# Performance work log

Hardware: AMD Instinct MI355X
Metric: run time of the kernel (lower is better)

## Reference

```python
import jax, jax.numpy as jnp
import numpy as np

B, L, D, H = 32, 512, 512, 8          # batch(=num_nodes), seq len, model_size, num_heads
HD = D // H                            # head size
E_DIM, N_EDGES, N_PATHS = 128, 4096, 1024  # edge_dim (hardcoded 128), edge table, #(src,dst) pairs
MAXD = H                               # max_path_distance == num_heads


def setup_inputs() -> dict:
    rng = jax.random.key(0)
    ks = jax.random.split(rng, 16)
    n = lambda k, s: jax.random.normal(k, s, jnp.float32)
    idx = jnp.arange(N_PATHS)
    inp = {
        'query': n(ks[0], (B, L, D)),
        'key':   n(ks[1], (B, L, D)),
        'value': n(ks[2], (B, L, D)),
        'mask':  jnp.ones((B, 1, 1, L), jnp.float32),
        'edge_attr': n(ks[3], (N_EDGES, E_DIM)),
        'path_src': (idx // B).astype(jnp.int32),   # all (src,dst) node pairs
        'path_dst': (idx % B).astype(jnp.int32),
        'path_edges': jax.random.randint(ks[4], (N_PATHS, MAXD), 0, N_EDGES),
        'path_lens': jax.random.randint(ks[5], (N_PATHS,), 1, MAXD + 1),
        # learned params
        'WQ': n(ks[6], (D, D)) * 0.02, 'bQ': jnp.zeros((D,), jnp.float32),
        'WK': n(ks[7], (D, D)) * 0.02, 'bK': jnp.zeros((D,), jnp.float32),
        'WV': n(ks[8], (D, D)) * 0.02, 'bV': jnp.zeros((D,), jnp.float32),
        'WO': n(ks[9], (D, D)) * 0.02, 'bO': jnp.zeros((D,), jnp.float32),
        'edge_vector': n(ks[10], (MAXD, E_DIM)) * 0.05,  # EdgeEncoding weight
        'b_vec': n(ks[11], (MAXD,)) * 0.05,              # SpatialEncoding weight
        'b_scale': jnp.float32(0.001),
        'c_scale': jnp.float32(0.001),
    }
    return inp


def reference(query, key, value, mask, edge_attr, path_src, path_dst, path_edges,
              path_lens, WQ, bQ, WK, bK, WV, bV, WO, bO, edge_vector, b_vec,
              b_scale, c_scale):
    def split_heads(x):  # [B,L,D] -> [B,H,L,HD]
        return x.reshape(B, L, H, HD).transpose(0, 2, 1, 3)

    q = split_heads(jnp.einsum('bld,de->ble', query, WQ) + bQ)
    k = split_heads(jnp.einsum('bld,de->ble', key, WK) + bK)
    v = split_heads(jnp.einsum('bld,de->ble', value, WV) + bV)

    score = jnp.einsum('bhqd,bhkd->bhqk', q, k) / jnp.sqrt(jnp.float32(HD))

    pl = jnp.minimum(path_lens, MAXD).astype(jnp.int32)  # clipped path lengths

    # SpatialEncoding: spatial[src,dst] = b_vec[min(len,maxd)-1]
    spatial = jnp.zeros((B, B), jnp.float32).at[path_src, path_dst].set(b_vec[pl - 1])
    b_mean = spatial.mean(axis=1)  # [B]

    # EdgeEncoding: cij[src,dst] = mean_k <edge_vector[k], edge_attr[path[k]]>
    pe = edge_attr[path_edges]                       # [P,MAXD,E]  batched gather
    dots = jnp.einsum('ke,pke->pk', edge_vector, pe)  # [P,MAXD]
    kmask = (jnp.arange(MAXD)[None, :] < pl[:, None]).astype(jnp.float32)
    cvals = jnp.where(pl > 0, (dots * kmask).sum(1) / jnp.maximum(pl, 1), 0.0)
    cij = jnp.zeros((B, B), jnp.float32).at[path_src, path_dst].set(cvals)
    c_mean = cij.mean(axis=1)  # [B]

    bias = (b_scale * b_mean + c_scale * c_mean)[:, None, None, None]
    score = score + bias + (1.0 - mask) * (-1e9)

    alpha = jax.nn.softmax(score, axis=-1)
    ctx = jnp.einsum('bhqk,bhkd->bhqd', alpha, v)
    ctx = ctx.transpose(0, 2, 1, 3).reshape(B, L, D)
    return jnp.einsum('bld,de->ble', ctx, WO) + bO
```

## Files before the change

kernel.cpp:

```cpp
#include <hip/hip_runtime.h>
#include <hip/hip_bf16.h>

#define B_  32
#define L_  512
#define D_  512
#define H_  8
#define HD_ 64

typedef __attribute__((ext_vector_type(8))) short bf16x8;
typedef __attribute__((ext_vector_type(4))) short bf16x4;
typedef __attribute__((ext_vector_type(4))) float f32x4;

__device__ __forceinline__ short f2bf(float f) {
  union { float f; unsigned u; } x; x.f = f;
  unsigned r = x.u + 0x7FFFu + ((x.u >> 16) & 1u);
  return (short)(r >> 16);
}

__device__ __forceinline__ void gll16(const void* g, void* l) {
  __builtin_amdgcn_global_load_lds(
      (const __attribute__((address_space(1))) unsigned int*)g,
      (__attribute__((address_space(3))) unsigned int*)l, 16, 0, 0);
}

__device__ __forceinline__ bf16x8 cvt8(f32x4 a, f32x4 b) {
  union { __hip_bfloat162 h[4]; bf16x8 v; } u;
  u.h[0] = __float22bfloat162_rn(float2{a[0], a[1]});
  u.h[1] = __float22bfloat162_rn(float2{a[2], a[3]});
  u.h[2] = __float22bfloat162_rn(float2{b[0], b[1]});
  u.h[3] = __float22bfloat162_rn(float2{b[2], b[3]});
  return u.v;
}

#define DS_FENCE() do { asm volatile("s_waitcnt lgkmcnt(0)" ::: "memory"); \
                        __builtin_amdgcn_sched_barrier(0); } while (0)

__global__ __launch_bounds__(256) void wt_kernel(
    const float* __restrict__ WQ, const float* __restrict__ WK,
    const float* __restrict__ WV, const float* __restrict__ WO,
    short* __restrict__ wt) {
  __shared__ float tile[32][33];
  int wz = blockIdx.z;
  const float* W = (wz == 0) ? WQ : (wz == 1) ? WK : (wz == 2) ? WV : WO;
  int k0 = blockIdx.y * 32, n0 = blockIdx.x * 32;
  int tr = threadIdx.x >> 5, tc = threadIdx.x & 31;
#pragma unroll
  for (int i = 0; i < 4; ++i)
    tile[tr + i * 8][tc] = W[(size_t)(k0 + tr + i * 8) * D_ + n0 + tc];
  __syncthreads();
#pragma unroll
  for (int i = 0; i < 4; ++i)
    wt[((size_t)wz * D_ + n0 + tr + i * 8) * D_ + k0 + tc] =
        f2bf(tile[tc][tr + i * 8]);
}

__global__ __launch_bounds__(256, 4) void gemm_qkv(
    const float* __restrict__ Xq, const float* __restrict__ Xk,
    const float* __restrict__ Xv, const short* __restrict__ wt,
    const float* __restrict__ bQ, const float* __restrict__ bK,
    const float* __restrict__ bV,
    short* __restrict__ q_ws, short* __restrict__ k_ws,
    short* __restrict__ vt_ws) {
  __shared__ __align__(16) char lds[32768];
  char* Al = lds;
  char* Bl = lds + 16384;

  int mode = blockIdx.z;
  const float* A = (mode == 0) ? Xq : (mode == 1) ? Xk : Xv;
  const short* WT = wt + (size_t)mode * D_ * D_;
  const float* bias = (mode == 0) ? bQ : (mode == 1) ? bK : bV;

  int wgid = blockIdx.x + 4 * blockIdx.y;
  int xcd = wgid & 7, idx = wgid >> 3;
  int m0 = (xcd * 32 + (idx >> 2)) * 64;
  int n0 = (idx & 3) * 128;

  int tid = threadIdx.x, lane = tid & 63, w = tid >> 6;
  int wr = w >> 1, wc = w & 1, g = lane >> 4, lr = lane & 15;

  f32x4 acc[2][4] = {};

#pragma unroll
  for (int ks = 0; ks < 8; ++ks) {
    __syncthreads();
#pragma unroll
    for (int j = 0; j < 4; ++j) {
      int e = w * 4 + j;
      int row = e * 4 + (lane >> 4);
      int chunk = (lane & 15) ^ (row & 15);
      gll16(A + (size_t)(m0 + row) * D_ + ks * 64 + chunk * 4, Al + e * 1024);
    }
#pragma unroll
    for (int j = 0; j < 4; ++j) {
      int e = w * 4 + j;
      int row = e * 8 + (lane >> 3);
      int chunk = (lane & 7) ^ (lane >> 3);
      gll16(WT + (size_t)(n0 + row) * D_ + ks * 64 + chunk * 8, Bl + e * 1024);
    }
    __syncthreads();
#pragma unroll
    for (int kk = 0; kk < 2; ++kk) {
      bf16x8 af[2], bf_[4];
#pragma unroll
      for (int i = 0; i < 2; ++i) {
        int row = wr * 32 + i * 16 + lr;
        int o0 = ((kk * 8 + g * 2) ^ lr) << 4;
        int o1 = ((kk * 8 + g * 2 + 1) ^ lr) << 4;
        f32x4 lo = *(const f32x4*)(Al + row * 256 + o0);
        f32x4 hi = *(const f32x4*)(Al + row * 256 + o1);
        af[i] = cvt8(lo, hi);
      }
#pragma unroll
      for (int i = 0; i < 4; ++i) {
        int row = wc * 64 + i * 16 + lr;
        bf_[i] = *(const bf16x8*)(Bl + row * 128 +
                                  (((kk * 4 + g) ^ (lr & 7)) << 4));
      }
#pragma unroll
      for (int mi = 0; mi < 2; ++mi)
#pragma unroll
        for (int nj = 0; nj < 4; ++nj)
          acc[mi][nj] = __builtin_amdgcn_mfma_f32_16x16x32_bf16(
              af[mi], bf_[nj], acc[mi][nj], 0, 0, 0);
    }
  }

#pragma unroll
  for (int mi = 0; mi < 2; ++mi) {
#pragma unroll
    for (int nj = 0; nj < 4; ++nj) {
      int n = n0 + wc * 64 + nj * 16 + lr;
      float bb = bias[n];
      int h = n >> 6, hd = n & 63;
#pragma unroll
      for (int rr = 0; rr < 4; ++rr) {
        int m = m0 + wr * 32 + mi * 16 + g * 4 + rr;
        int b = m >> 9, l = m & 511;
        short v = f2bf(acc[mi][nj][rr] + bb);
        if (mode == 0)
          q_ws[(((size_t)b * H_ + h) * L_ + l) * HD_ + hd] = v;
        else if (mode == 1)
          k_ws[(((size_t)b * H_ + h) * L_ + l) * HD_ + hd] = v;
        else
          vt_ws[(((size_t)b * H_ + h) * HD_ + hd) * L_ + l] = v;
      }
    }
  }
}

__global__ __launch_bounds__(256, 4) void attn_kernel(
    const short* __restrict__ q_ws, const short* __restrict__ k_ws,
    const short* __restrict__ vt_ws, const float* __restrict__ mask,
    short* __restrict__ ctx_ws) {
  __shared__ __align__(16) char lds[40960];
  int wg = blockIdx.x;
  int bh   = (wg & 7) * 32 + (wg >> 6);
  int qblk = (wg >> 3) & 7;
  int b = bh >> 3, h = bh & 7;
  int tid = threadIdx.x, lane = tid & 63, w = tid >> 6;
  int g = lane >> 4, lr = lane & 15;
  char* Pl = lds + 32768 + w * 2048;
  int qbase = qblk * 64 + w * 16;

  const short* Qh  = q_ws  + (size_t)bh * (L_ * HD_);
  const short* Kh  = k_ws  + (size_t)bh * (L_ * HD_);
  const short* VTh = vt_ws + (size_t)bh * (HD_ * L_);
  const float* mrow = mask + (size_t)b * L_;

  bf16x8 aq0 = *(const bf16x8*)(Qh + (size_t)(qbase + lr) * HD_ + g * 8);
  bf16x8 aq1 = *(const bf16x8*)(Qh + (size_t)(qbase + lr) * HD_ + 32 + g * 8);

  float mb_all[32];
#pragma unroll
  for (int ch = 0; ch < 8; ++ch)
#pragma unroll
    for (int kt = 0; kt < 4; ++kt)
      mb_all[ch * 4 + kt] = (1.0f - mrow[ch * 64 + kt * 16 + lr]) * -1e9f;

  int rowin = lane >> 3;
  int sch8 = ((lane & 7) ^ rowin) * 8;

#pragma unroll
  for (int j = 0; j < 2; ++j) {
    int e = w * 2 + j, row = e * 8 + rowin;
    gll16(Kh + (size_t)row * HD_ + sch8, lds + e * 1024);
    gll16(VTh + (size_t)row * L_ + sch8, lds + 16384 + e * 1024);
  }
  __syncthreads();

  f32x4 c[4] = {};
  float m[4] = {-1e30f, -1e30f, -1e30f, -1e30f};
  float sum[4] = {0.f, 0.f, 0.f, 0.f};

#pragma unroll
  for (int ch = 0; ch < 8; ++ch) {
    const char* Kb = lds + (ch & 1) * 8192;
    const char* Vb = lds + 16384 + (ch & 1) * 8192;
    if (ch < 7) {
      char* Kn = lds + ((ch + 1) & 1) * 8192;
      char* Vn = lds + 16384 + ((ch + 1) & 1) * 8192;
#pragma unroll
      for (int j = 0; j < 2; ++j) {
        int e = w * 2 + j, row = e * 8 + rowin;
        gll16(Kh + ((size_t)(ch + 1) * 64 + row) * HD_ + sch8, Kn + e * 1024);
        gll16(VTh + (size_t)row * L_ + (ch + 1) * 64 + sch8, Vn + e * 1024);
      }
    }

    f32x4 s[4];
    __builtin_amdgcn_s_setprio(1);
#pragma unroll
    for (int kt = 0; kt < 4; ++kt) {
      int row = kt * 16 + lr;
      bf16x8 bk0 = *(const bf16x8*)(Kb + row * 128 + ((g ^ (lr & 7)) << 4));
      bf16x8 bk1 = *(const bf16x8*)(Kb + row * 128 + (((4 + g) ^ (lr & 7)) << 4));
      f32x4 a = {0.f, 0.f, 0.f, 0.f};
      a = __builtin_amdgcn_mfma_f32_16x16x32_bf16(aq0, bk0, a, 0, 0, 0);
      a = __builtin_amdgcn_mfma_f32_16x16x32_bf16(aq1, bk1, a, 0, 0, 0);
#pragma unroll
      for (int rr = 0; rr < 4; ++rr)
        a[rr] = a[rr] * 0.125f + mb_all[ch * 4 + kt];
      s[kt] = a;
    }
    __builtin_amdgcn_s_setprio(0);

    float pmax[4];
#pragma unroll
    for (int rr = 0; rr < 4; ++rr)
      pmax[rr] = fmaxf(fmaxf(s[0][rr], s[1][rr]), fmaxf(s[2][rr], s[3][rr]));
#pragma unroll
    for (int off = 1; off < 16; off <<= 1)
#pragma unroll
      for (int rr = 0; rr < 4; ++rr)
        pmax[rr] = fmaxf(pmax[rr], __shfl_xor(pmax[rr], off, 64));

    int ok = (pmax[0] - m[0] <= 8.f) & (pmax[1] - m[1] <= 8.f) &
             (pmax[2] - m[2] <= 8.f) & (pmax[3] - m[3] <= 8.f);
    if (!__all(ok)) {
      float scl[4];
#pragma unroll
      for (int rr = 0; rr < 4; ++rr) {
        float mn = fmaxf(m[rr], pmax[rr]);
        scl[rr] = __expf(m[rr] - mn);
        m[rr] = mn;
        sum[rr] *= scl[rr];
      }
#pragma unroll
      for (int nt = 0; nt < 4; ++nt)
#pragma unroll
        for (int rr = 0; rr < 4; ++rr) c[nt][rr] *= scl[rr];
    }

#pragma unroll
    for (int kt = 0; kt < 4; ++kt) {
      int col2 = (kt * 16 + lr) * 2;
#pragma unroll
      for (int rr = 0; rr < 4; ++rr) {
        float p = __expf(s[kt][rr] - m[rr]);
        sum[rr] += p;
        int row = g * 4 + rr;
        *(short*)(Pl + row * 128 + (col2 ^ ((row & 7) << 4))) = f2bf(p);
      }
    }
    DS_FENCE();

    __builtin_amdgcn_s_setprio(1);
#pragma unroll
    for (int kk = 0; kk < 2; ++kk) {
      bf16x8 ap = *(const bf16x8*)(Pl + lr * 128 +
                                   (((kk * 4 + g) ^ (lr & 7)) << 4));
#pragma unroll
      for (int nt = 0; nt < 4; ++nt) {
        int row = nt * 16 + lr;
        bf16x8 bv = *(const bf16x8*)(Vb + row * 128 +
                                     (((kk * 4 + g) ^ (lr & 7)) << 4));
        c[nt] = __builtin_amdgcn_mfma_f32_16x16x32_bf16(ap, bv, c[nt], 0, 0, 0);
      }
    }
    __builtin_amdgcn_s_setprio(0);
    DS_FENCE();
    if (ch < 7) __syncthreads();
  }

  float inv[4];
#pragma unroll
  for (int off = 1; off < 16; off <<= 1)
#pragma unroll
    for (int rr = 0; rr < 4; ++rr) sum[rr] += __shfl_xor(sum[rr], off, 64);
#pragma unroll
  for (int rr = 0; rr < 4; ++rr) inv[rr] = 1.0f / sum[rr];

#pragma unroll
  for (int nt = 0; nt < 4; ++nt) {
    int hd = nt * 16 + lr;
#pragma unroll
    for (int rr = 0; rr < 4; ++rr) {
      int qrow = qbase + g * 4 + rr;
      ctx_ws[(((size_t)b * L_ + qrow) * H_ + h) * HD_ + hd] =
          f2bf(c[nt][rr] * inv[rr]);
    }
  }
}

__global__ __launch_bounds__(256, 4) void gemm_out(
    const short* __restrict__ ctx, const short* __restrict__ wt3,
    const float* __restrict__ bO, float* __restrict__ out) {
  __shared__ __align__(16) char lds[24576];
  char* Al = lds;
  char* Bl = lds + 8192;
  int wgid = blockIdx.x + 4 * blockIdx.y;
  int xcd = wgid & 7, idx = wgid >> 3;
  int m0 = (xcd * 32 + (idx >> 2)) * 64;
  int n0 = (idx & 3) * 128;
  int tid = threadIdx.x, lane = tid & 63, w = tid >> 6;
  int wr = w >> 1, wc = w & 1, g = lane >> 4, lr = lane & 15;

  f32x4 acc[2][4] = {};

#pragma unroll
  for (int ks = 0; ks < 8; ++ks) {
    __syncthreads();
#pragma unroll
    for (int j = 0; j < 2; ++j) {
      int e = w * 2 + j;
      int row = e * 8 + (lane >> 3);
      int chunk = (lane & 7) ^ (lane >> 3);
      gll16(ctx + (size_t)(m0 + row) * D_ + ks * 64 + chunk * 8, Al + e * 1024);
    }
#pragma unroll
    for (int j = 0; j < 4; ++j) {
      int e = w * 4 + j;
      int row = e * 8 + (lane >> 3);
      int chunk = (lane & 7) ^ (lane >> 3);
      gll16(wt3 + (size_t)(n0 + row) * D_ + ks * 64 + chunk * 8, Bl + e * 1024);
    }
    __syncthreads();
#pragma unroll
    for (int kk = 0; kk < 2; ++kk) {
      bf16x8 af[2], bf_[4];
#pragma unroll
      for (int i = 0; i < 2; ++i) {
        int row = wr * 32 + i * 16 + lr;
        af[i] = *(const bf16x8*)(Al + row * 128 +
                                 (((kk * 4 + g) ^ (lr & 7)) << 4));
      }
#pragma unroll
      for (int i = 0; i < 4; ++i) {
        int row = wc * 64 + i * 16 + lr;
        bf_[i] = *(const bf16x8*)(Bl + row * 128 +
                                  (((kk * 4 + g) ^ (lr & 7)) << 4));
      }
#pragma unroll
      for (int mi = 0; mi < 2; ++mi)
#pragma unroll
        for (int nj = 0; nj < 4; ++nj)
          acc[mi][nj] = __builtin_amdgcn_mfma_f32_16x16x32_bf16(
              af[mi], bf_[nj], acc[mi][nj], 0, 0, 0);
    }
  }
#pragma unroll
  for (int mi = 0; mi < 2; ++mi) {
#pragma unroll
    for (int nj = 0; nj < 4; ++nj) {
      int n = n0 + wc * 64 + nj * 16 + lr;
      float bb = bO[n];
#pragma unroll
      for (int rr = 0; rr < 4; ++rr) {
        int m = m0 + wr * 32 + mi * 16 + g * 4 + rr;
        out[(size_t)m * D_ + n] = acc[mi][nj][rr] + bb;
      }
    }
  }
}

extern "C" void kernel_launch(void* const* d_in, const int* in_sizes, int n_in,
                              void* d_out, int out_size, void* d_ws,
                              size_t ws_size, hipStream_t stream) {
  const float* query = (const float*)d_in[0];
  const float* key   = (const float*)d_in[1];
  const float* value = (const float*)d_in[2];
  const float* mask  = (const float*)d_in[3];
  const float* WQ = (const float*)d_in[9];
  const float* bQ = (const float*)d_in[10];
  const float* WK = (const float*)d_in[11];
  const float* bK = (const float*)d_in[12];
  const float* WV = (const float*)d_in[13];
  const float* bV = (const float*)d_in[14];
  const float* WO = (const float*)d_in[15];
  const float* bO = (const float*)d_in[16];

  short* ws  = (short*)d_ws;
  short* wt  = ws;
  short* q   = ws + 1048576;
  short* k   = q + 8388608;
  short* vt  = k + 8388608;
  short* ctx = vt + 8388608;
  float* out = (float*)d_out;

  wt_kernel<<<dim3(16, 16, 4), 256, 0, stream>>>(WQ, WK, WV, WO, wt);
  gemm_qkv<<<dim3(4, 256, 3), 256, 0, stream>>>(query, key, value, wt,
                                                bQ, bK, bV, q, k, vt);
  attn_kernel<<<2048, 256, 0, stream>>>(q, k, vt, mask, ctx);
  gemm_out<<<dim3(4, 256), 256, 0, stream>>>(ctx, wt + 3 * 262144, bO, out);
}
```

Measured before the change: 130.9 us.

## Load QKV GEMM A operand directly to registers with register prefetch

The fp32 activation tile in the QKV projection GEMM is no longer staged through LDS. Each lane now loads its A fragment straight from global memory into registers and prefetches the next k-step while the current one computes. This removes the A-side LDS traffic and halves the LDS footprint, which may allow higher occupancy. In exchange it uses more registers, and the per-lane global loads are less coalesced, since rows are read by different lanes and each row is read by both column-warps.

```diff
diff --git a/kernel.cpp b/kernel.cpp
--- a/kernel.cpp
+++ b/kernel.cpp
@@ -61,9 +61,7 @@
     const float* __restrict__ bV,
     short* __restrict__ q_ws, short* __restrict__ k_ws,
     short* __restrict__ vt_ws) {
-  __shared__ __align__(16) char lds[32768];
-  char* Al = lds;
-  char* Bl = lds + 16384;
+  __shared__ __align__(16) char Bl[16384];
 
   int mode = blockIdx.z;
   const float* A = (mode == 0) ? Xq : (mode == 1) ? Xk : Xv;
@@ -78,17 +76,37 @@
   int tid = threadIdx.x, lane = tid & 63, w = tid >> 6;
   int wr = w >> 1, wc = w & 1, g = lane >> 4, lr = lane & 15;
 
+  const float* Ab = A + (size_t)(m0 + wr * 32 + lr) * D_ + g * 8;
+
+  f32x4 ar[2][2][2];
+#pragma unroll
+  for (int i = 0; i < 2; ++i)
+#pragma unroll
+    for (int kk = 0; kk < 2; ++kk) {
+      ar[i][kk][0] = *(const f32x4*)(Ab + i * 16 * D_ + kk * 32);
+      ar[i][kk][1] = *(const f32x4*)(Ab + i * 16 * D_ + kk * 32 + 4);
+    }
+
   f32x4 acc[2][4] = {};
 
 #pragma unroll
   for (int ks = 0; ks < 8; ++ks) {
     __syncthreads();
-#pragma unroll
-    for (int j = 0; j < 4; ++j) {
-      int e = w * 4 + j;
-      int row = e * 4 + (lane >> 4);
-      int chunk = (lane & 15) ^ (row & 15);
-      gll16(A + (size_t)(m0 + row) * D_ + ks * 64 + chunk * 4, Al + e * 1024);
+    bf16x8 af[2][2];
+#pragma unroll
+    for (int i = 0; i < 2; ++i)
+#pragma unroll
+      for (int kk = 0; kk < 2; ++kk)
+        af[i][kk] = cvt8(ar[i][kk][0], ar[i][kk][1]);
+    if (ks < 7) {
+#pragma unroll
+      for (int i = 0; i < 2; ++i)
+#pragma unroll
+        for (int kk = 0; kk < 2; ++kk) {
+          const float* p = Ab + i * 16 * D_ + (ks + 1) * 64 + kk * 32;
+          ar[i][kk][0] = *(const f32x4*)p;
+          ar[i][kk][1] = *(const f32x4*)(p + 4);
+        }
     }
 #pragma unroll
     for (int j = 0; j < 4; ++j) {
@@ -100,16 +118,7 @@
     __syncthreads();
 #pragma unroll
     for (int kk = 0; kk < 2; ++kk) {
-      bf16x8 af[2], bf_[4];
-#pragma unroll
-      for (int i = 0; i < 2; ++i) {
-        int row = wr * 32 + i * 16 + lr;
-        int o0 = ((kk * 8 + g * 2) ^ lr) << 4;
-        int o1 = ((kk * 8 + g * 2 + 1) ^ lr) << 4;
-        f32x4 lo = *(const f32x4*)(Al + row * 256 + o0);
-        f32x4 hi = *(const f32x4*)(Al + row * 256 + o1);
-        af[i] = cvt8(lo, hi);
-      }
+      bf16x8 bf_[4];
 #pragma unroll
       for (int i = 0; i < 4; ++i) {
         int row = wc * 64 + i * 16 + lr;
@@ -121,7 +130,7 @@
 #pragma unroll
         for (int nj = 0; nj < 4; ++nj)
           acc[mi][nj] = __builtin_amdgcn_mfma_f32_16x16x32_bf16(
-              af[mi], bf_[nj], acc[mi][nj], 0, 0, 0);
+              af[mi][kk], bf_[nj], acc[mi][nj], 0, 0, 0);
     }
   }
 
```

After: 189.6 us. 1.45x slower.
